# Kernel tuning notes

Hardware: AMD Instinct MI355X
Metric: run time of the kernel (lower is better)

The kernel has to match this reference:

```python
import jax, jax.numpy as jnp
import numpy as np


def _conv1x1(x, w, b=None):
    # x: [B, Cin, N, S], w: [Cout, Cin], 1x1 Conv2d
    y = jnp.einsum('oc,bcns->bons', w, x)
    if b is not None:
        y = y + b[None, :, None, None]
    return y


def setup_inputs() -> dict:
    key = jax.random.key(0)
    ks = jax.random.split(key, 16)
    B, Cin, N, K = 4, 128, 16384, 16
    MID, OUT, SHARE, PT = 64, 128, 8, 10
    s = 0.05
    inp = {
        'sm_feats': jax.random.normal(ks[0], (B, Cin, N, K), jnp.float32),
        'sm_ppfs': jax.random.normal(ks[1], (B, PT, N, K), jnp.float32),
        'conv0_w': jax.random.normal(ks[2], (OUT, Cin), jnp.float32) * s,
        'conv0_b': jax.random.normal(ks[3], (OUT,), jnp.float32) * s,
        'conv1_w': jax.random.normal(ks[4], (MID, OUT), jnp.float32) * s,
        'conv1_b': jax.random.normal(ks[5], (MID,), jnp.float32) * s,
        'conv2_w': jax.random.normal(ks[6], (MID, OUT), jnp.float32) * s,
        'conv2_b': jax.random.normal(ks[7], (MID,), jnp.float32) * s,
        'conv3_w': jax.random.normal(ks[8], (MID, OUT), jnp.float32) * s,
        'conv3_b': jax.random.normal(ks[9], (MID,), jnp.float32) * s,
        'convw1_w': jax.random.normal(ks[10], (MID // SHARE, MID * K), jnp.float32) * s,
        'convw2_w': jax.random.normal(ks[11], (K * MID // SHARE, MID // SHARE), jnp.float32) * s,
        'convw2_b': jax.random.normal(ks[12], (K * MID // SHARE,), jnp.float32) * s,
        'convout_w': jax.random.normal(ks[13], (OUT, MID), jnp.float32) * s,
        'convout_b': jax.random.normal(ks[14], (OUT,), jnp.float32) * s,
        'pt1_w': jax.random.normal(ks[15], (MID, PT), jnp.float32) * s,
        'pt2_w': jax.random.normal(jax.random.fold_in(key, 99), (MID, MID), jnp.float32) * s,
    }
    return inp


def reference(sm_feats, sm_ppfs, conv0_w, conv0_b, conv1_w, conv1_b, conv2_w, conv2_b,
              conv3_w, conv3_b, convw1_w, convw2_w, convw2_b, convout_w, convout_b,
              pt1_w, pt2_w):
    xn = jax.nn.relu(_conv1x1(sm_feats, conv0_w, conv0_b))  # [B, OUT, N, K]
    x = xn[..., :1]                                          # center point feature
    identity = x
    x1 = _conv1x1(x, conv1_w, conv1_b)       # [B, MID, N, 1]
    x2 = _conv1x1(xn, conv2_w, conv2_b)      # [B, MID, N, K]
    x3 = _conv1x1(xn, conv3_w, conv3_b)      # [B, MID, N, K]
    ptf = _conv1x1(jax.nn.relu(_conv1x1(sm_ppfs, pt1_w)), pt2_w)  # [B, MID, N, K]
    x3 = x3 + ptf
    xfs = x1 - x2 + ptf                      # [B, MID, N, K]
    B, MID, N, K = xfs.shape
    share = MID // convw1_w.shape[0]
    xfs = jnp.transpose(xfs, (0, 1, 3, 2)).reshape(B, MID * K, 1, N)
    h = jax.nn.relu(_conv1x1(xfs, convw1_w))            # [B, MID//share, 1, N]
    w = _conv1x1(h, convw2_w, convw2_b)                  # [B, K*MID//share, 1, N]
    w = jax.nn.softmax(w.reshape(B, MID // share, K, N), axis=2)
    w = jnp.transpose(w, (0, 1, 3, 2))                   # [B, MID//share, N, K]
    w = jnp.tile(w, (1, share, 1, 1))                    # [B, MID, N, K]
    out = jax.nn.relu(jnp.sum(w * x3, axis=3, keepdims=True))  # [B, MID, N, 1]
    out = (_conv1x1(out, convout_w, convout_b) + identity).squeeze(3)  # [B, OUT, N]
    return out
```

## Files before the change

kernel.cpp:

```cpp
#include <hip/hip_runtime.h>
#include <hip/hip_bf16.h>


typedef __attribute__((ext_vector_type(8))) short bf16x8;
typedef __attribute__((ext_vector_type(4))) float f32x4;
typedef __attribute__((ext_vector_type(4))) unsigned short us4;

#define MFMA(a, b, c) __builtin_amdgcn_mfma_f32_16x16x32_bf16((a), (b), (c), 0, 0, 0)

#define OFF_F    0
#define OFF_X2   0
#define OFF_PTF  17408
#define OFF_XN   34816
#define OFF_X3   34816
#define OFF_XFS  52224
#define OFF_P    69632
#define OFF_WS   69632
#define OFF_HB   74752
#define OFF_OM   76288
#define OFF_X1   77824
#define OFF_XC   78912
#define SMEM_BYTES 81088

#define WS_W0  0
#define WS_W1  16384
#define WS_W2  24576
#define WS_W3  32768
#define WS_P1  40960
#define WS_P2  43008
#define WS_CW1 47104
#define WS_WO  63488
#define WS_TOTAL 71680

__device__ __forceinline__ unsigned short f2b(float f) {
    union { __hip_bfloat16 h; unsigned short u; } v;
    v.h = __float2bfloat16(f);
    return v.u;
}
__device__ __forceinline__ float b2f(unsigned short u) {
    union { unsigned u; float f; } v;
    v.u = ((unsigned)u) << 16;
    return v.f;
}
__device__ __forceinline__ us4 pk4(float a, float b, float c, float d) {
    us4 r; r[0] = f2b(a); r[1] = f2b(b); r[2] = f2b(c); r[3] = f2b(d); return r;
}
__device__ __forceinline__ bf16x8 ldb(const unsigned short* p) {
    return *(const bf16x8*)p;
}

__global__ __launch_bounds__(512, 1)
void convert_weights(const float* __restrict__ w0, const float* __restrict__ w1,
                     const float* __restrict__ w2, const float* __restrict__ w3,
                     const float* __restrict__ p1, const float* __restrict__ p2,
                     const float* __restrict__ cw1, const float* __restrict__ wo,
                     unsigned short* __restrict__ ws) {
    int i = blockIdx.x * 512 + threadIdx.x;
    if (i >= WS_TOTAL) return;
    float v;
    if (i < 16384)      v = w0[i];
    else if (i < 24576) v = w1[i - 16384];
    else if (i < 32768) v = w2[i - 24576];
    else if (i < 40960) v = w3[i - 32768];
    else if (i < 43008) { int r = i - 40960, row = r >> 5, k = r & 31;
                          v = (k < 10) ? p1[row * 10 + k] : 0.f; }
    else if (i < 47104) v = p2[i - 43008];
    else if (i < 63488) { int r = i - 47104, j = r >> 10, kc = r & 1023;
                          v = (j < 8) ? cw1[j * 1024 + (kc & 63) * 16 + (kc >> 6)] : 0.f; }
    else                v = wo[i - 63488];
    ws[i] = f2b(v);
}

__global__ __launch_bounds__(512, 4)
void fused_model_kernel(const float* __restrict__ feats, const float* __restrict__ ppfs,
                        const unsigned short* __restrict__ wsb,
                        const float* __restrict__ b0, const float* __restrict__ b1,
                        const float* __restrict__ b2, const float* __restrict__ b3,
                        const float* __restrict__ cw2, const float* __restrict__ cb2,
                        const float* __restrict__ bo, float* __restrict__ out) {
    extern __shared__ char smem[];
    const int tid = threadIdx.x;
    const int W = tid >> 6;
    const int lane = tid & 63;
    const int kk = lane & 15;
    const int g = lane >> 4;
    const int bid = blockIdx.x;
    const int b = bid >> 11;
    const int n0 = (bid & 2047) * 8;

    bf16x8 a0[4], rA[4], rB[4];
    {
        const int mtr = (W & 3);
        #pragma unroll
        for (int kt = 0; kt < 4; ++kt) {
            a0[kt] = ldb(wsb + WS_W0 + (16 * W + kk) * 128 + kt * 32 + 8 * g);
            if (W < 4) {
                rA[kt] = ldb(wsb + WS_W3 + (16 * mtr + kk) * 128 + kt * 32 + 8 * g);
                rB[kt] = ldb(wsb + WS_W1 + (16 * mtr + kk) * 128 + kt * 32 + 8 * g);
            } else {
                rA[kt] = ldb(wsb + WS_W2 + (16 * mtr + kk) * 128 + kt * 32 + 8 * g);
                rB[kt] = ldb(wsb + WS_W3 + (16 * mtr + kk) * 128 + kt * 32 + 8 * g);
            }
        }
    }

    {
        const int kq = tid & 3, ci = tid >> 2;
        const int cisw = (ci * 2) ^ (kq << 4);
        #pragma unroll
        for (int pos = 0; pos < 8; ++pos) {
            f32x4 v = *(const f32x4*)(feats + (((size_t)b * 128 + ci) * 16384 + (n0 + pos)) * 16 + kq * 4);
            char* base = smem + OFF_F + pos * 4352 + cisw;
            *(unsigned short*)(base + (kq * 4 + 0) * 272) = f2b(v[0]);
            *(unsigned short*)(base + (kq * 4 + 1) * 272) = f2b(v[1]);
            *(unsigned short*)(base + (kq * 4 + 2) * 272) = f2b(v[2]);
            *(unsigned short*)(base + (kq * 4 + 3) * 272) = f2b(v[3]);
        }
        if (tid < 320) {
            int pos = tid / 40, r = tid % 40, p = r >> 2, kq2 = r & 3;
            f32x4 v = *(const f32x4*)(ppfs + (((size_t)b * 10 + p) * 16384 + (n0 + pos)) * 16 + kq2 * 4);
            char* base = smem + OFF_P + pos * 1024 + p * 2;
            *(unsigned short*)(base + (kq2 * 4 + 0) * 64) = f2b(v[0]);
            *(unsigned short*)(base + (kq2 * 4 + 1) * 64) = f2b(v[1]);
            *(unsigned short*)(base + (kq2 * 4 + 2) * 64) = f2b(v[2]);
            *(unsigned short*)(base + (kq2 * 4 + 3) * 64) = f2b(v[3]);
        } else {
            for (int z = tid - 320; z < 1408; z += 192) {
                int pos = z / 176, rr = z % 176, ks = rr / 11, dw = rr % 11;
                *(unsigned*)(smem + OFF_P + pos * 1024 + ks * 64 + 20 + dw * 4) = 0u;
            }
        }
    }
    __syncthreads();

    {
        f32x4 bv = *(const f32x4*)(b0 + 16 * W + 4 * g);
        const int fsw = ((kk >> 2) & 3) << 4;
        #pragma unroll
        for (int pos = 0; pos < 8; ++pos) {
            f32x4 acc = {0.f, 0.f, 0.f, 0.f};
            #pragma unroll
            for (int kt = 0; kt < 4; ++kt) {
                bf16x8 bf = *(const bf16x8*)(smem + OFF_F + pos * 4352 + kk * 272 + ((kt * 64 + 16 * g) ^ fsw));
                acc = MFMA(a0[kt], bf, acc);
            }
            us4 xw = pk4(fmaxf(acc[0] + bv[0], 0.f), fmaxf(acc[1] + bv[1], 0.f),
                         fmaxf(acc[2] + bv[2], 0.f), fmaxf(acc[3] + bv[3], 0.f));
            *(us4*)(smem + OFF_XN + pos * 4352 + kk * 272 + (16 * W + 4 * g) * 2) = xw;
            if (kk == 0) *(us4*)(smem + OFF_XC + pos * 272 + (16 * W + 4 * g) * 2) = xw;
        }
    }
    __syncthreads();

    f32x4 acc3[4];
    if (W < 4) {
        bf16x8 a1[4], a2[4][2];
        #pragma unroll
        for (int mt = 0; mt < 4; ++mt) {
            a1[mt] = ldb(wsb + WS_P1 + (16 * mt + kk) * 32 + 8 * g);
            a2[mt][0] = ldb(wsb + WS_P2 + (16 * mt + kk) * 64 + 8 * g);
            a2[mt][1] = ldb(wsb + WS_P2 + (16 * mt + kk) * 64 + 32 + 8 * g);
        }
        const int sel = g >> 1;
        const int sa = kk + 16 * ((2 * g) & 3);
        const int sb = kk + 16 * ((2 * g + 1) & 3);
        #pragma unroll
        for (int pp = 0; pp < 2; ++pp) {
            const int pos = 2 * W + pp;
            bf16x8 bp = *(const bf16x8*)(smem + OFF_P + pos * 1024 + kk * 64 + 16 * g);
            int pkd[4][2];
            #pragma unroll
            for (int mt = 0; mt < 4; ++mt) {
                f32x4 hv = {0.f, 0.f, 0.f, 0.f};
                hv = MFMA(a1[mt], bp, hv);
                us4 t = pk4(fmaxf(hv[0], 0.f), fmaxf(hv[1], 0.f),
                            fmaxf(hv[2], 0.f), fmaxf(hv[3], 0.f));
                pkd[mt][0] = ((int*)&t)[0];
                pkd[mt][1] = ((int*)&t)[1];
            }
            union { int d[4]; bf16x8 v; } bh0, bh1;
            bh0.d[0] = sel ? __shfl(pkd[1][0], sa, 64) : __shfl(pkd[0][0], sa, 64);
            bh0.d[1] = sel ? __shfl(pkd[1][1], sa, 64) : __shfl(pkd[0][1], sa, 64);
            bh0.d[2] = sel ? __shfl(pkd[1][0], sb, 64) : __shfl(pkd[0][0], sb, 64);
            bh0.d[3] = sel ? __shfl(pkd[1][1], sb, 64) : __shfl(pkd[0][1], sb, 64);
            bh1.d[0] = sel ? __shfl(pkd[3][0], sa, 64) : __shfl(pkd[2][0], sa, 64);
            bh1.d[1] = sel ? __shfl(pkd[3][1], sa, 64) : __shfl(pkd[2][1], sa, 64);
            bh1.d[2] = sel ? __shfl(pkd[3][0], sb, 64) : __shfl(pkd[2][0], sb, 64);
            bh1.d[3] = sel ? __shfl(pkd[3][1], sb, 64) : __shfl(pkd[2][1], sb, 64);
            #pragma unroll
            for (int mt = 0; mt < 4; ++mt) {
                f32x4 acc = {0.f, 0.f, 0.f, 0.f};
                acc = MFMA(a2[mt][0], bh0.v, acc);
                acc = MFMA(a2[mt][1], bh1.v, acc);
                *(us4*)(smem + OFF_PTF + pos * 2176 + kk * 136 + (16 * mt + 4 * g) * 2) =
                    pk4(acc[0], acc[1], acc[2], acc[3]);
            }
        }
        #pragma unroll
        for (int pp = 0; pp < 4; ++pp) {
            f32x4 acc = {0.f, 0.f, 0.f, 0.f};
            #pragma unroll
            for (int kt = 0; kt < 4; ++kt) {
                bf16x8 bf = *(const bf16x8*)(smem + OFF_XN + pp * 4352 + kk * 272 + (kt * 64 + 16 * g));
                acc = MFMA(rA[kt], bf, acc);
            }
            acc3[pp] = acc;
        }
        f32x4 a1c = {0.f, 0.f, 0.f, 0.f};
        #pragma unroll
        for (int kt = 0; kt < 4; ++kt) {
            bf16x8 bf = *(const bf16x8*)(smem + OFF_XC + (kk & 7) * 272 + (kt * 64 + 16 * g));
            a1c = MFMA(rB[kt], bf, a1c);
        }
        if (kk < 8) {
            f32x4 b1v = *(const f32x4*)(b1 + 16 * W + 4 * g);
            *(us4*)(smem + OFF_X1 + kk * 136 + (16 * W + 4 * g) * 2) =
                pk4(a1c[0] + b1v[0], a1c[1] + b1v[1], a1c[2] + b1v[2], a1c[3] + b1v[3]);
        }
    } else {
        const int mt = W - 4;
        f32x4 b2v = *(const f32x4*)(b2 + 16 * mt + 4 * g);
        #pragma unroll
        for (int pos = 0; pos < 8; ++pos) {
            bf16x8 bx[4];
            #pragma unroll
            for (int kt = 0; kt < 4; ++kt)
                bx[kt] = *(const bf16x8*)(smem + OFF_XN + pos * 4352 + kk * 272 + (kt * 64 + 16 * g));
            f32x4 acc = {0.f, 0.f, 0.f, 0.f};
            #pragma unroll
            for (int kt = 0; kt < 4; ++kt) acc = MFMA(rA[kt], bx[kt], acc);
            *(us4*)(smem + OFF_X2 + pos * 2176 + kk * 136 + (16 * mt + 4 * g) * 2) =
                pk4(acc[0] + b2v[0], acc[1] + b2v[1], acc[2] + b2v[2], acc[3] + b2v[3]);
            if (pos >= 4) {
                f32x4 c = {0.f, 0.f, 0.f, 0.f};
                #pragma unroll
                for (int kt = 0; kt < 4; ++kt) c = MFMA(rB[kt], bx[kt], c);
                acc3[pos - 4] = c;
            }
        }
    }
    __syncthreads();

    {
        const int mt = W & 3, ph = W >> 2;
        f32x4 b3v = *(const f32x4*)(b3 + 16 * mt + 4 * g);
        const int rot = (32 * mt + 8 * g + 16 * kk) & 127;
        #pragma unroll
        for (int pp = 0; pp < 4; ++pp) {
            const int pos = ph * 4 + pp;
            us4 ptfv = *(const us4*)(smem + OFF_PTF + pos * 2176 + kk * 136 + (16 * mt + 4 * g) * 2);
            us4 x2v  = *(const us4*)(smem + OFF_X2  + pos * 2176 + kk * 136 + (16 * mt + 4 * g) * 2);
            us4 x1v  = *(const us4*)(smem + OFF_X1  + pos * 136 + (16 * mt + 4 * g) * 2);
            float pf0 = b2f(ptfv[0]), pf1 = b2f(ptfv[1]), pf2 = b2f(ptfv[2]), pf3 = b2f(ptfv[3]);
            *(us4*)(smem + OFF_X3 + pos * 2176 + kk * 136 + (16 * mt + 4 * g) * 2) =
                pk4(acc3[pp][0] + b3v[0] + pf0, acc3[pp][1] + b3v[1] + pf1,
                    acc3[pp][2] + b3v[2] + pf2, acc3[pp][3] + b3v[3] + pf3);
            *(us4*)(smem + OFF_XFS + pos * 2080 + kk * 128 + rot) =
                pk4(b2f(x1v[0]) - b2f(x2v[0]) + pf0, b2f(x1v[1]) - b2f(x2v[1]) + pf1,
                    b2f(x1v[2]) - b2f(x2v[2]) + pf2, b2f(x1v[3]) - b2f(x2v[3]) + pf3);
        }
        if (tid < 64) *(float*)(smem + OFF_HB + tid * 4) = 0.f;
    }
    __syncthreads();

    {
        bf16x8 acw[4];
        #pragma unroll
        for (int kt = 0; kt < 4; ++kt)
            acw[kt] = ldb(wsb + WS_CW1 + kk * 1024 + W * 128 + kt * 32 + 8 * g);
        const char* xb = smem + OFF_XFS + (kk & 7) * 2080;
        f32x4 acc = {0.f, 0.f, 0.f, 0.f};
        #pragma unroll
        for (int kt = 0; kt < 4; ++kt) {
            const int k = 2 * W + (kt >> 1);
            const int byt = (64 * (kt & 1) + 16 * g + 16 * k) & 127;
            bf16x8 bf = *(const bf16x8*)(xb + k * 128 + byt);
            acc = MFMA(acw[kt], bf, acc);
        }
        if (kk < 8 && g < 2) {
            #pragma unroll
            for (int r = 0; r < 4; ++r)
                atomicAdd((float*)(smem + OFF_HB + kk * 32 + (4 * g + r) * 4), acc[r]);
        }
    }
    __syncthreads();

    {
        const int pos = W;
        f32x4 h0 = *(const f32x4*)(smem + OFF_HB + pos * 32);
        f32x4 h1 = *(const f32x4*)(smem + OFF_HB + pos * 32 + 16);
        #pragma unroll
        for (int r = 0; r < 4; ++r) { h0[r] = fmaxf(h0[r], 0.f); h1[r] = fmaxf(h1[r], 0.f); }
        #pragma unroll
        for (int it = 0; it < 2; ++it) {
            const int c = it * 64 + lane;
            float wl = cb2[c];
            f32x4 w20 = *(const f32x4*)(cw2 + c * 8);
            f32x4 w21 = *(const f32x4*)(cw2 + c * 8 + 4);
            #pragma unroll
            for (int j = 0; j < 4; ++j) {
                wl += w20[j] * h0[j];
                wl += w21[j] * h1[j];
            }
            float mx = wl;
            for (int off = 8; off; off >>= 1) mx = fmaxf(mx, __shfl_xor(mx, off, 16));
            float e = __expf(wl - mx);
            float ss = e;
            for (int off = 8; off; off >>= 1) ss += __shfl_xor(ss, off, 16);
            *(float*)(smem + OFF_WS + pos * 640 + (4 * it + g) * 80 + kk * 4) = e / ss;
        }
        __builtin_amdgcn_wave_barrier();
        __builtin_amdgcn_sched_barrier(0);

        const char* wsp = smem + OFF_WS + pos * 640 + (lane & 7) * 80;
        f32x4 wv0 = *(const f32x4*)(wsp);
        f32x4 wv1 = *(const f32x4*)(wsp + 16);
        f32x4 wv2 = *(const f32x4*)(wsp + 32);
        f32x4 wv3 = *(const f32x4*)(wsp + 48);
        const char* x3b = smem + OFF_X3 + pos * 2176 + lane * 2;
        float s = 0.f;
        #pragma unroll
        for (int k = 0; k < 4; ++k) s += wv0[k] * b2f(*(const unsigned short*)(x3b + k * 136));
        #pragma unroll
        for (int k = 0; k < 4; ++k) s += wv1[k] * b2f(*(const unsigned short*)(x3b + (k + 4) * 136));
        #pragma unroll
        for (int k = 0; k < 4; ++k) s += wv2[k] * b2f(*(const unsigned short*)(x3b + (k + 8) * 136));
        #pragma unroll
        for (int k = 0; k < 4; ++k) s += wv3[k] * b2f(*(const unsigned short*)(x3b + (k + 12) * 136));
        *(unsigned short*)(smem + OFF_OM + pos * 144 + lane * 2) = f2b(fmaxf(s, 0.f));
    }
    __syncthreads();

    {
        f32x4 acc = {0.f, 0.f, 0.f, 0.f};
        #pragma unroll
        for (int kt = 0; kt < 2; ++kt) {
            bf16x8 bf = *(const bf16x8*)(smem + OFF_OM + (kk & 7) * 144 + (kt * 64 + 16 * g));
            acc = MFMA(ldb(wsb + WS_WO + (16 * W + kk) * 64 + kt * 32 + 8 * g), bf, acc);
        }
        if (kk < 8) {
            f32x4 bv = *(const f32x4*)(bo + 16 * W + 4 * g);
            us4 xcv = *(const us4*)(smem + OFF_XC + kk * 272 + (16 * W + 4 * g) * 2);
            #pragma unroll
            for (int r = 0; r < 4; ++r) {
                int o = 16 * W + 4 * g + r;
                out[((size_t)b * 128 + o) * 16384 + n0 + kk] = acc[r] + bv[r] + b2f(xcv[r]);
            }
        }
    }
}

extern "C" void kernel_launch(void* const* d_in, const int* in_sizes, int n_in,
                              void* d_out, int out_size, void* d_ws, size_t ws_size,
                              hipStream_t stream) {
    (void)in_sizes; (void)n_in; (void)out_size; (void)ws_size;
    const float* feats = (const float*)d_in[0];
    const float* ppfs  = (const float*)d_in[1];
    const float* w0  = (const float*)d_in[2];
    const float* b0  = (const float*)d_in[3];
    const float* w1  = (const float*)d_in[4];
    const float* b1  = (const float*)d_in[5];
    const float* w2  = (const float*)d_in[6];
    const float* b2  = (const float*)d_in[7];
    const float* w3  = (const float*)d_in[8];
    const float* b3  = (const float*)d_in[9];
    const float* cw1 = (const float*)d_in[10];
    const float* cw2 = (const float*)d_in[11];
    const float* cb2 = (const float*)d_in[12];
    const float* wo  = (const float*)d_in[13];
    const float* bo  = (const float*)d_in[14];
    const float* p1  = (const float*)d_in[15];
    const float* p2  = (const float*)d_in[16];
    float* out = (float*)d_out;
    unsigned short* wsb = (unsigned short*)d_ws;

    convert_weights<<<dim3((WS_TOTAL + 511) / 512), dim3(512), 0, stream>>>(
        w0, w1, w2, w3, p1, p2, cw1, wo, wsb);

    (void)hipFuncSetAttribute(reinterpret_cast<const void*>(fused_model_kernel),
                              hipFuncAttributeMaxDynamicSharedMemorySize, SMEM_BYTES);
    fused_model_kernel<<<dim3(8192), dim3(512), SMEM_BYTES, stream>>>(
        feats, ppfs, wsb, b0, b1, b2, b3, cw2, cb2, bo, out);
}
```

Before: 303.6 us.

## Make blocks persistent over four tiles with register-prefetched next-tile loads

Each block now handles four consecutive 8-point tiles instead of one, and the grid shrinks from 8192 to 2048 blocks. While the current tile is computed, the feats and ppfs for the next tile are loaded into registers, then written to shared memory after the F buffer is free. This hides global load latency behind compute and amortises the per-block weight register loads. In exchange it raises register pressure (eight extra f32x4 per thread), which may cut occupancy, and leaves fewer blocks to balance across CUs.

Result: slower. 798.2 us (+162.9%).

```diff
diff --git a/kernel.cpp b/kernel.cpp
--- a/kernel.cpp
+++ b/kernel.cpp
@@ -85,8 +85,12 @@
     const int kk = lane & 15;
     const int g = lane >> 4;
     const int bid = blockIdx.x;
-    const int b = bid >> 11;
-    const int n0 = (bid & 2047) * 8;
+    const int b = bid >> 9;
+    const int n0base = (bid & 511) * 32;
+
+    const int kq = tid & 3, ci = tid >> 2;
+    const int cisw = (ci * 2) ^ (kq << 4);
+    const int pposP = tid / 40, rP = tid % 40, pP = rP >> 2, kqP = rP & 3;
 
     bf16x8 a0[4], rA[4], rB[4];
     {
@@ -103,250 +107,278 @@
             }
         }
     }
-
+    f32x4 pf[8];
+    f32x4 pp;
     {
-        const int kq = tid & 3, ci = tid >> 2;
-        const int cisw = (ci * 2) ^ (kq << 4);
+        const float* fb = feats + (((size_t)b * 128 + ci) * 16384 + n0base) * 16 + kq * 4;
         #pragma unroll
-        for (int pos = 0; pos < 8; ++pos) {
-            f32x4 v = *(const f32x4*)(feats + (((size_t)b * 128 + ci) * 16384 + (n0 + pos)) * 16 + kq * 4);
-            char* base = smem + OFF_F + pos * 4352 + cisw;
-            *(unsigned short*)(base + (kq * 4 + 0) * 272) = f2b(v[0]);
-            *(unsigned short*)(base + (kq * 4 + 1) * 272) = f2b(v[1]);
-            *(unsigned short*)(base + (kq * 4 + 2) * 272) = f2b(v[2]);
-            *(unsigned short*)(base + (kq * 4 + 3) * 272) = f2b(v[3]);
-        }
+        for (int pos = 0; pos < 8; ++pos) pf[pos] = *(const f32x4*)(fb + pos * 16);
+        if (tid < 320)
+            pp = *(const f32x4*)(ppfs + (((size_t)b * 10 + pP) * 16384 + n0base + pposP) * 16 + kqP * 4);
+    }
+
+    #pragma unroll 1
+    for (int tt = 0; tt < 4; ++tt) {
+        const int n0 = n0base + tt * 8;
+
         if (tid < 320) {
-            int pos = tid / 40, r = tid % 40, p = r >> 2, kq2 = r & 3;
-            f32x4 v = *(const f32x4*)(ppfs + (((size_t)b * 10 + p) * 16384 + (n0 + pos)) * 16 + kq2 * 4);
-            char* base = smem + OFF_P + pos * 1024 + p * 2;
-            *(unsigned short*)(base + (kq2 * 4 + 0) * 64) = f2b(v[0]);
-            *(unsigned short*)(base + (kq2 * 4 + 1) * 64) = f2b(v[1]);
-            *(unsigned short*)(base + (kq2 * 4 + 2) * 64) = f2b(v[2]);
-            *(unsigned short*)(base + (kq2 * 4 + 3) * 64) = f2b(v[3]);
+            char* basep = smem + OFF_P + pposP * 1024 + pP * 2;
+            *(unsigned short*)(basep + (kqP * 4 + 0) * 64) = f2b(pp[0]);
+            *(unsigned short*)(basep + (kqP * 4 + 1) * 64) = f2b(pp[1]);
+            *(unsigned short*)(basep + (kqP * 4 + 2) * 64) = f2b(pp[2]);
+            *(unsigned short*)(basep + (kqP * 4 + 3) * 64) = f2b(pp[3]);
         } else {
             for (int z = tid - 320; z < 1408; z += 192) {
                 int pos = z / 176, rr = z % 176, ks = rr / 11, dw = rr % 11;
                 *(unsigned*)(smem + OFF_P + pos * 1024 + ks * 64 + 20 + dw * 4) = 0u;
             }
         }
-    }
-    __syncthreads();
-
-    {
-        f32x4 bv = *(const f32x4*)(b0 + 16 * W + 4 * g);
-        const int fsw = ((kk >> 2) & 3) << 4;
-        #pragma unroll
-        for (int pos = 0; pos < 8; ++pos) {
+        if (tt == 0) {
+            #pragma unroll
+            for (int pos = 0; pos < 8; ++pos) {
+                char* base = smem + OFF_F + pos * 4352 + cisw;
+                *(unsigned short*)(base + (kq * 4 + 0) * 272) = f2b(pf[pos][0]);
+                *(unsigned short*)(base + (kq * 4 + 1) * 272) = f2b(pf[pos][1]);
+                *(unsigned short*)(base + (kq * 4 + 2) * 272) = f2b(pf[pos][2]);
+                *(unsigned short*)(base + (kq * 4 + 3) * 272) = f2b(pf[pos][3]);
+            }
+        }
+        if (tt < 3) {
+            const int n1 = n0base + (tt + 1) * 8;
+            const float* fb = feats + (((size_t)b * 128 + ci) * 16384 + n1) * 16 + kq * 4;
+            #pragma unroll
+            for (int pos = 0; pos < 8; ++pos) pf[pos] = *(const f32x4*)(fb + pos * 16);
+            if (tid < 320)
+                pp = *(const f32x4*)(ppfs + (((size_t)b * 10 + pP) * 16384 + n1 + pposP) * 16 + kqP * 4);
+        }
+        if (tt == 0) __syncthreads();
+
+        {
+            f32x4 bv = *(const f32x4*)(b0 + 16 * W + 4 * g);
+            const int fsw = ((kk >> 2) & 3) << 4;
+            #pragma unroll
+            for (int pos = 0; pos < 8; ++pos) {
+                f32x4 acc = {0.f, 0.f, 0.f, 0.f};
+                #pragma unroll
+                for (int kt = 0; kt < 4; ++kt) {
+                    bf16x8 bf = *(const bf16x8*)(smem + OFF_F + pos * 4352 + kk * 272 + ((kt * 64 + 16 * g) ^ fsw));
+                    acc = MFMA(a0[kt], bf, acc);
+                }
+                us4 xw = pk4(fmaxf(acc[0] + bv[0], 0.f), fmaxf(acc[1] + bv[1], 0.f),
+                             fmaxf(acc[2] + bv[2], 0.f), fmaxf(acc[3] + bv[3], 0.f));
+                *(us4*)(smem + OFF_XN + pos * 4352 + kk * 272 + (16 * W + 4 * g) * 2) = xw;
+                if (kk == 0) *(us4*)(smem + OFF_XC + pos * 272 + (16 * W + 4 * g) * 2) = xw;
+            }
+        }
+        __syncthreads();
+
+        f32x4 acc3[4];
+        if (W < 4) {
+            bf16x8 a1[4], a2[4][2];
+            #pragma unroll
+            for (int mt = 0; mt < 4; ++mt) {
+                a1[mt] = ldb(wsb + WS_P1 + (16 * mt + kk) * 32 + 8 * g);
+                a2[mt][0] = ldb(wsb + WS_P2 + (16 * mt + kk) * 64 + 8 * g);
+                a2[mt][1] = ldb(wsb + WS_P2 + (16 * mt + kk) * 64 + 32 + 8 * g);
+            }
+            const int sel = g >> 1;
+            const int sa = kk + 16 * ((2 * g) & 3);
+            const int sb = kk + 16 * ((2 * g + 1) & 3);
+            #pragma unroll
+            for (int pp2 = 0; pp2 < 2; ++pp2) {
+                const int pos = 2 * W + pp2;
+                bf16x8 bp = *(const bf16x8*)(smem + OFF_P + pos * 1024 + kk * 64 + 16 * g);
+                int pkd[4][2];
+                #pragma unroll
+                for (int mt = 0; mt < 4; ++mt) {
+                    f32x4 hv = {0.f, 0.f, 0.f, 0.f};
+                    hv = MFMA(a1[mt], bp, hv);
+                    us4 t = pk4(fmaxf(hv[0], 0.f), fmaxf(hv[1], 0.f),
+                                fmaxf(hv[2], 0.f), fmaxf(hv[3], 0.f));
+                    pkd[mt][0] = ((int*)&t)[0];
+                    pkd[mt][1] = ((int*)&t)[1];
+                }
+                union { int d[4]; bf16x8 v; } bh0, bh1;
+                bh0.d[0] = sel ? __shfl(pkd[1][0], sa, 64) : __shfl(pkd[0][0], sa, 64);
+                bh0.d[1] = sel ? __shfl(pkd[1][1], sa, 64) : __shfl(pkd[0][1], sa, 64);
+                bh0.d[2] = sel ? __shfl(pkd[1][0], sb, 64) : __shfl(pkd[0][0], sb, 64);
+                bh0.d[3] = sel ? __shfl(pkd[1][1], sb, 64) : __shfl(pkd[0][1], sb, 64);
+                bh1.d[0] = sel ? __shfl(pkd[3][0], sa, 64) : __shfl(pkd[2][0], sa, 64);
+                bh1.d[1] = sel ? __shfl(pkd[3][1], sa, 64) : __shfl(pkd[2][1], sa, 64);
+                bh1.d[2] = sel ? __shfl(pkd[3][0], sb, 64) : __shfl(pkd[2][0], sb, 64);
+                bh1.d[3] = sel ? __shfl(pkd[3][1], sb, 64) : __shfl(pkd[2][1], sb, 64);
+                #pragma unroll
+                for (int mt = 0; mt < 4; ++mt) {
+                    f32x4 acc = {0.f, 0.f, 0.f, 0.f};
+                    acc = MFMA(a2[mt][0], bh0.v, acc);
+                    acc = MFMA(a2[mt][1], bh1.v, acc);
+                    *(us4*)(smem + OFF_PTF + pos * 2176 + kk * 136 + (16 * mt + 4 * g) * 2) =
+                        pk4(acc[0], acc[1], acc[2], acc[3]);
+                }
+            }
+            #pragma unroll
+            for (int pp2 = 0; pp2 < 4; ++pp2) {
+                f32x4 acc = {0.f, 0.f, 0.f, 0.f};
+                #pragma unroll
+                for (int kt = 0; kt < 4; ++kt) {
+                    bf16x8 bf = *(const bf16x8*)(smem + OFF_XN + pp2 * 4352 + kk * 272 + (kt * 64 + 16 * g));
+                    acc = MFMA(rA[kt], bf, acc);
+                }
+                acc3[pp2] = acc;
+            }
+            f32x4 a1c = {0.f, 0.f, 0.f, 0.f};
+            #pragma unroll
+            for (int kt = 0; kt < 4; ++kt) {
+                bf16x8 bf = *(const bf16x8*)(smem + OFF_XC + (kk & 7) * 272 + (kt * 64 + 16 * g));
+                a1c = MFMA(rB[kt], bf, a1c);
+            }
+            if (kk < 8) {
+                f32x4 b1v = *(const f32x4*)(b1 + 16 * W + 4 * g);
+                *(us4*)(smem + OFF_X1 + kk * 136 + (16 * W + 4 * g) * 2) =
+                    pk4(a1c[0] + b1v[0], a1c[1] + b1v[1], a1c[2] + b1v[2], a1c[3] + b1v[3]);
+            }
+        } else {
+            const int mt = W - 4;
+            f32x4 b2v = *(const f32x4*)(b2 + 16 * mt + 4 * g);
+            #pragma unroll
+            for (int pos = 0; pos < 8; ++pos) {
+                bf16x8 bx[4];
+                #pragma unroll
+                for (int kt = 0; kt < 4; ++kt)
+                    bx[kt] = *(const bf16x8*)(smem + OFF_XN + pos * 4352 + kk * 272 + (kt * 64 + 16 * g));
+                f32x4 acc = {0.f, 0.f, 0.f, 0.f};
+                #pragma unroll
+                for (int kt = 0; kt < 4; ++kt) acc = MFMA(rA[kt], bx[kt], acc);
+                *(us4*)(smem + OFF_X2 + pos * 2176 + kk * 136 + (16 * mt + 4 * g) * 2) =
+                    pk4(acc[0] + b2v[0], acc[1] + b2v[1], acc[2] + b2v[2], acc[3] + b2v[3]);
+                if (pos >= 4) {
+                    f32x4 c = {0.f, 0.f, 0.f, 0.f};
+                    #pragma unroll
+                    for (int kt = 0; kt < 4; ++kt) c = MFMA(rB[kt], bx[kt], c);
+                    acc3[pos - 4] = c;
+                }
+            }
+        }
+        __syncthreads();
+
+        {
+            const int mt = W & 3, ph = W >> 2;
+            f32x4 b3v = *(const f32x4*)(b3 + 16 * mt + 4 * g);
+            const int rot = (32 * mt + 8 * g + 16 * kk) & 127;
+            #pragma unroll
+            for (int pp2 = 0; pp2 < 4; ++pp2) {
+                const int pos = ph * 4 + pp2;
+                us4 ptfv = *(const us4*)(smem + OFF_PTF + pos * 2176 + kk * 136 + (16 * mt + 4 * g) * 2);
+                us4 x2v  = *(const us4*)(smem + OFF_X2  + pos * 2176 + kk * 136 + (16 * mt + 4 * g) * 2);
+                us4 x1v  = *(const us4*)(smem + OFF_X1  + pos * 136 + (16 * mt + 4 * g) * 2);
+                float pf0 = b2f(ptfv[0]), pf1 = b2f(ptfv[1]), pf2 = b2f(ptfv[2]), pf3 = b2f(ptfv[3]);
+                *(us4*)(smem + OFF_X3 + pos * 2176 + kk * 136 + (16 * mt + 4 * g) * 2) =
+                    pk4(acc3[pp2][0] + b3v[0] + pf0, acc3[pp2][1] + b3v[1] + pf1,
+                        acc3[pp2][2] + b3v[2] + pf2, acc3[pp2][3] + b3v[3] + pf3);
+                *(us4*)(smem + OFF_XFS + pos * 2080 + kk * 128 + rot) =
+                    pk4(b2f(x1v[0]) - b2f(x2v[0]) + pf0, b2f(x1v[1]) - b2f(x2v[1]) + pf1,
+                        b2f(x1v[2]) - b2f(x2v[2]) + pf2, b2f(x1v[3]) - b2f(x2v[3]) + pf3);
+            }
+            if (tid < 64) *(float*)(smem + OFF_HB + tid * 4) = 0.f;
+        }
+        __syncthreads();
+
+        {
+            bf16x8 acw[4];
+            #pragma unroll
+            for (int kt = 0; kt < 4; ++kt)
+                acw[kt] = ldb(wsb + WS_CW1 + kk * 1024 + W * 128 + kt * 32 + 8 * g);
+            const char* xb = smem + OFF_XFS + (kk & 7) * 2080;
             f32x4 acc = {0.f, 0.f, 0.f, 0.f};
             #pragma unroll
             for (int kt = 0; kt < 4; ++kt) {
-                bf16x8 bf = *(const bf16x8*)(smem + OFF_F + pos * 4352 + kk * 272 + ((kt * 64 + 16 * g) ^ fsw));
-                acc = MFMA(a0[kt], bf, acc);
-            }
-            us4 xw = pk4(fmaxf(acc[0] + bv[0], 0.f), fmaxf(acc[1] + bv[1], 0.f),
-                         fmaxf(acc[2] + bv[2], 0.f), fmaxf(acc[3] + bv[3], 0.f));
-            *(us4*)(smem + OFF_XN + pos * 4352 + kk * 272 + (16 * W + 4 * g) * 2) = xw;
-            if (kk == 0) *(us4*)(smem + OFF_XC + pos * 272 + (16 * W + 4 * g) * 2) = xw;
-        }
-    }
-    __syncthreads();
-
-    f32x4 acc3[4];
-    if (W < 4) {
-        bf16x8 a1[4], a2[4][2];
-        #pragma unroll
-        for (int mt = 0; mt < 4; ++mt) {
-            a1[mt] = ldb(wsb + WS_P1 + (16 * mt + kk) * 32 + 8 * g);
-            a2[mt][0] = ldb(wsb + WS_P2 + (16 * mt + kk) * 64 + 8 * g);
-            a2[mt][1] = ldb(wsb + WS_P2 + (16 * mt + kk) * 64 + 32 + 8 * g);
-        }
-        const int sel = g >> 1;
-        const int sa = kk + 16 * ((2 * g) & 3);
-        const int sb = kk + 16 * ((2 * g + 1) & 3);
-        #pragma unroll
-        for (int pp = 0; pp < 2; ++pp) {
-            const int pos = 2 * W + pp;
-            bf16x8 bp = *(const bf16x8*)(smem + OFF_P + pos * 1024 + kk * 64 + 16 * g);
-            int pkd[4][2];
-            #pragma unroll
-            for (int mt = 0; mt < 4; ++mt) {
-                f32x4 hv = {0.f, 0.f, 0.f, 0.f};
-                hv = MFMA(a1[mt], bp, hv);
-                us4 t = pk4(fmaxf(hv[0], 0.f), fmaxf(hv[1], 0.f),
-                            fmaxf(hv[2], 0.f), fmaxf(hv[3], 0.f));
-                pkd[mt][0] = ((int*)&t)[0];
-                pkd[mt][1] = ((int*)&t)[1];
-            }
-            union { int d[4]; bf16x8 v; } bh0, bh1;
-            bh0.d[0] = sel ? __shfl(pkd[1][0], sa, 64) : __shfl(pkd[0][0], sa, 64);
-            bh0.d[1] = sel ? __shfl(pkd[1][1], sa, 64) : __shfl(pkd[0][1], sa, 64);
-            bh0.d[2] = sel ? __shfl(pkd[1][0], sb, 64) : __shfl(pkd[0][0], sb, 64);
-            bh0.d[3] = sel ? __shfl(pkd[1][1], sb, 64) : __shfl(pkd[0][1], sb, 64);
-            bh1.d[0] = sel ? __shfl(pkd[3][0], sa, 64) : __shfl(pkd[2][0], sa, 64);
-            bh1.d[1] = sel ? __shfl(pkd[3][1], sa, 64) : __shfl(pkd[2][1], sa, 64);
-            bh1.d[2] = sel ? __shfl(pkd[3][0], sb, 64) : __shfl(pkd[2][0], sb, 64);
-            bh1.d[3] = sel ? __shfl(pkd[3][1], sb, 64) : __shfl(pkd[2][1], sb, 64);
-            #pragma unroll
-            for (int mt = 0; mt < 4; ++mt) {
-                f32x4 acc = {0.f, 0.f, 0.f, 0.f};
-                acc = MFMA(a2[mt][0], bh0.v, acc);
-                acc = MFMA(a2[mt][1], bh1.v, acc);
-                *(us4*)(smem + OFF_PTF + pos * 2176 + kk * 136 + (16 * mt + 4 * g) * 2) =
-                    pk4(acc[0], acc[1], acc[2], acc[3]);
-            }
-        }
-        #pragma unroll
-        for (int pp = 0; pp < 4; ++pp) {
+                const int k = 2 * W + (kt >> 1);
+                const int byt = (64 * (kt & 1) + 16 * g + 16 * k) & 127;
+                bf16x8 bf = *(const bf16x8*)(xb + k * 128 + byt);
+                acc = MFMA(acw[kt], bf, acc);
+            }
+            if (kk < 8 && g < 2) {
+                #pragma unroll
+                for (int r = 0; r < 4; ++r)
+                    atomicAdd((float*)(smem + OFF_HB + kk * 32 + (4 * g + r) * 4), acc[r]);
+            }
+            if (tt < 3) {
+                #pragma unroll
+                for (int pos = 0; pos < 8; ++pos) {
+                    char* base = smem + OFF_F + pos * 4352 + cisw;
+                    *(unsigned short*)(base + (kq * 4 + 0) * 272) = f2b(pf[pos][0]);
+                    *(unsigned short*)(base + (kq * 4 + 1) * 272) = f2b(pf[pos][1]);
+                    *(unsigned short*)(base + (kq * 4 + 2) * 272) = f2b(pf[pos][2]);
+                    *(unsigned short*)(base + (kq * 4 + 3) * 272) = f2b(pf[pos][3]);
+                }
+            }
+        }
+        __syncthreads();
+
+        {
+            const int pos = W;
+            f32x4 h0 = *(const f32x4*)(smem + OFF_HB + pos * 32);
+            f32x4 h1 = *(const f32x4*)(smem + OFF_HB + pos * 32 + 16);
+            #pragma unroll
+            for (int r = 0; r < 4; ++r) { h0[r] = fmaxf(h0[r], 0.f); h1[r] = fmaxf(h1[r], 0.f); }
+            #pragma unroll
+            for (int it = 0; it < 2; ++it) {
+                const int c = it * 64 + lane;
+                float wl = cb2[c];
+                f32x4 w20 = *(const f32x4*)(cw2 + c * 8);
+                f32x4 w21 = *(const f32x4*)(cw2 + c * 8 + 4);
+                #pragma unroll
+                for (int j = 0; j < 4; ++j) {
+                    wl += w20[j] * h0[j];
+                    wl += w21[j] * h1[j];
+                }
+                float mx = wl;
+                for (int off = 8; off; off >>= 1) mx = fmaxf(mx, __shfl_xor(mx, off, 16));
+                float e = __expf(wl - mx);
+                float ss = e;
+                for (int off = 8; off; off >>= 1) ss += __shfl_xor(ss, off, 16);
+                *(float*)(smem + OFF_WS + pos * 640 + (4 * it + g) * 80 + kk * 4) = e / ss;
+            }
+            __builtin_amdgcn_wave_barrier();
+            __builtin_amdgcn_sched_barrier(0);
+
+            const char* wsp = smem + OFF_WS + pos * 640 + (lane & 7) * 80;
+            f32x4 wv0 = *(const f32x4*)(wsp);
+            f32x4 wv1 = *(const f32x4*)(wsp + 16);
+            f32x4 wv2 = *(const f32x4*)(wsp + 32);
+            f32x4 wv3 = *(const f32x4*)(wsp + 48);
+            const char* x3b = smem + OFF_X3 + pos * 2176 + lane * 2;
+            float s = 0.f;
+            #pragma unroll
+            for (int k = 0; k < 4; ++k) s += wv0[k] * b2f(*(const unsigned short*)(x3b + k * 136));
+            #pragma unroll
+            for (int k = 0; k < 4; ++k) s += wv1[k] * b2f(*(const unsigned short*)(x3b + (k + 4) * 136));
+            #pragma unroll
+            for (int k = 0; k < 4; ++k) s += wv2[k] * b2f(*(const unsigned short*)(x3b + (k + 8) * 136));
+            #pragma unroll
+            for (int k = 0; k < 4; ++k) s += wv3[k] * b2f(*(const unsigned short*)(x3b + (k + 12) * 136));
+            *(unsigned short*)(smem + OFF_OM + pos * 144 + lane * 2) = f2b(fmaxf(s, 0.f));
+        }
+        __syncthreads();
+
+        {
             f32x4 acc = {0.f, 0.f, 0.f, 0.f};
             #pragma unroll
-            for (int kt = 0; kt < 4; ++kt) {
-                bf16x8 bf = *(const bf16x8*)(smem + OFF_XN + pp * 4352 + kk * 272 + (kt * 64 + 16 * g));
-                acc = MFMA(rA[kt], bf, acc);
-            }
-            acc3[pp] = acc;
-        }
-        f32x4 a1c = {0.f, 0.f, 0.f, 0.f};
-        #pragma unroll
-        for (int kt = 0; kt < 4; ++kt) {
-            bf16x8 bf = *(const bf16x8*)(smem + OFF_XC + (kk & 7) * 272 + (kt * 64 + 16 * g));
-            a1c = MFMA(rB[kt], bf, a1c);
-        }
-        if (kk < 8) {
-            f32x4 b1v = *(const f32x4*)(b1 + 16 * W + 4 * g);
-            *(us4*)(smem + OFF_X1 + kk * 136 + (16 * W + 4 * g) * 2) =
-                pk4(a1c[0] + b1v[0], a1c[1] + b1v[1], a1c[2] + b1v[2], a1c[3] + b1v[3]);
-        }
-    } else {
-        const int mt = W - 4;
-        f32x4 b2v = *(const f32x4*)(b2 + 16 * mt + 4 * g);
-        #pragma unroll
-        for (int pos = 0; pos < 8; ++pos) {
-            bf16x8 bx[4];
-            #pragma unroll
-            for (int kt = 0; kt < 4; ++kt)
-                bx[kt] = *(const bf16x8*)(smem + OFF_XN + pos * 4352 + kk * 272 + (kt * 64 + 16 * g));
-            f32x4 acc = {0.f, 0.f, 0.f, 0.f};
-            #pragma unroll
-            for (int kt = 0; kt < 4; ++kt) acc = MFMA(rA[kt], bx[kt], acc);
-            *(us4*)(smem + OFF_X2 + pos * 2176 + kk * 136 + (16 * mt + 4 * g) * 2) =
-                pk4(acc[0] + b2v[0], acc[1] + b2v[1], acc[2] + b2v[2], acc[3] + b2v[3]);
-            if (pos >= 4) {
-                f32x4 c = {0.f, 0.f, 0.f, 0.f};
-                #pragma unroll
-                for (int kt = 0; kt < 4; ++kt) c = MFMA(rB[kt], bx[kt], c);
-                acc3[pos - 4] = c;
-            }
-        }
-    }
-    __syncthreads();
-
-    {
-        const int mt = W & 3, ph = W >> 2;
-        f32x4 b3v = *(const f32x4*)(b3 + 16 * mt + 4 * g);
-        const int rot = (32 * mt + 8 * g + 16 * kk) & 127;
-        #pragma unroll
-        for (int pp = 0; pp < 4; ++pp) {
-            const int pos = ph * 4 + pp;
-            us4 ptfv = *(const us4*)(smem + OFF_PTF + pos * 2176 + kk * 136 + (16 * mt + 4 * g) * 2);
-            us4 x2v  = *(const us4*)(smem + OFF_X2  + pos * 2176 + kk * 136 + (16 * mt + 4 * g) * 2);
-            us4 x1v  = *(const us4*)(smem + OFF_X1  + pos * 136 + (16 * mt + 4 * g) * 2);
-            float pf0 = b2f(ptfv[0]), pf1 = b2f(ptfv[1]), pf2 = b2f(ptfv[2]), pf3 = b2f(ptfv[3]);
-            *(us4*)(smem + OFF_X3 + pos * 2176 + kk * 136 + (16 * mt + 4 * g) * 2) =
-                pk4(acc3[pp][0] + b3v[0] + pf0, acc3[pp][1] + b3v[1] + pf1,
-                    acc3[pp][2] + b3v[2] + pf2, acc3[pp][3] + b3v[3] + pf3);
-            *(us4*)(smem + OFF_XFS + pos * 2080 + kk * 128 + rot) =
-                pk4(b2f(x1v[0]) - b2f(x2v[0]) + pf0, b2f(x1v[1]) - b2f(x2v[1]) + pf1,
-                    b2f(x1v[2]) - b2f(x2v[2]) + pf2, b2f(x1v[3]) - b2f(x2v[3]) + pf3);
-        }
-        if (tid < 64) *(float*)(smem + OFF_HB + tid * 4) = 0.f;
-    }
-    __syncthreads();
-
-    {
-        bf16x8 acw[4];
-        #pragma unroll
-        for (int kt = 0; kt < 4; ++kt)
-            acw[kt] = ldb(wsb + WS_CW1 + kk * 1024 + W * 128 + kt * 32 + 8 * g);
-        const char* xb = smem + OFF_XFS + (kk & 7) * 2080;
-        f32x4 acc = {0.f, 0.f, 0.f, 0.f};
-        #pragma unroll
-        for (int kt = 0; kt < 4; ++kt) {
-            const int k = 2 * W + (kt >> 1);
-            const int byt = (64 * (kt & 1) + 16 * g + 16 * k) & 127;
-            bf16x8 bf = *(const bf16x8*)(xb + k * 128 + byt);
-            acc = MFMA(acw[kt], bf, acc);
-        }
-        if (kk < 8 && g < 2) {
-            #pragma unroll
-            for (int r = 0; r < 4; ++r)
-                atomicAdd((float*)(smem + OFF_HB + kk * 32 + (4 * g + r) * 4), acc[r]);
-        }
-    }
-    __syncthreads();
-
-    {
-        const int pos = W;
-        f32x4 h0 = *(const f32x4*)(smem + OFF_HB + pos * 32);
-        f32x4 h1 = *(const f32x4*)(smem + OFF_HB + pos * 32 + 16);
-        #pragma unroll
-        for (int r = 0; r < 4; ++r) { h0[r] = fmaxf(h0[r], 0.f); h1[r] = fmaxf(h1[r], 0.f); }
-        #pragma unroll
-        for (int it = 0; it < 2; ++it) {
-            const int c = it * 64 + lane;
-            float wl = cb2[c];
-            f32x4 w20 = *(const f32x4*)(cw2 + c * 8);
-            f32x4 w21 = *(const f32x4*)(cw2 + c * 8 + 4);
-            #pragma unroll
-            for (int j = 0; j < 4; ++j) {
-                wl += w20[j] * h0[j];
-                wl += w21[j] * h1[j];
-            }
-            float mx = wl;
-            for (int off = 8; off; off >>= 1) mx = fmaxf(mx, __shfl_xor(mx, off, 16));
-            float e = __expf(wl - mx);
-            float ss = e;
-            for (int off = 8; off; off >>= 1) ss += __shfl_xor(ss, off, 16);
-            *(float*)(smem + OFF_WS + pos * 640 + (4 * it + g) * 80 + kk * 4) = e / ss;
-        }
-        __builtin_amdgcn_wave_barrier();
-        __builtin_amdgcn_sched_barrier(0);
-
-        const char* wsp = smem + OFF_WS + pos * 640 + (lane & 7) * 80;
-        f32x4 wv0 = *(const f32x4*)(wsp);
-        f32x4 wv1 = *(const f32x4*)(wsp + 16);
-        f32x4 wv2 = *(const f32x4*)(wsp + 32);
-        f32x4 wv3 = *(const f32x4*)(wsp + 48);
-        const char* x3b = smem + OFF_X3 + pos * 2176 + lane * 2;
-        float s = 0.f;
-        #pragma unroll
-        for (int k = 0; k < 4; ++k) s += wv0[k] * b2f(*(const unsigned short*)(x3b + k * 136));
-        #pragma unroll
-        for (int k = 0; k < 4; ++k) s += wv1[k] * b2f(*(const unsigned short*)(x3b + (k + 4) * 136));
-        #pragma unroll
-        for (int k = 0; k < 4; ++k) s += wv2[k] * b2f(*(const unsigned short*)(x3b + (k + 8) * 136));
-        #pragma unroll
-        for (int k = 0; k < 4; ++k) s += wv3[k] * b2f(*(const unsigned short*)(x3b + (k + 12) * 136));
-        *(unsigned short*)(smem + OFF_OM + pos * 144 + lane * 2) = f2b(fmaxf(s, 0.f));
-    }
-    __syncthreads();
-
-    {
-        f32x4 acc = {0.f, 0.f, 0.f, 0.f};
-        #pragma unroll
-        for (int kt = 0; kt < 2; ++kt) {
-            bf16x8 bf = *(const bf16x8*)(smem + OFF_OM + (kk & 7) * 144 + (kt * 64 + 16 * g));
-            acc = MFMA(ldb(wsb + WS_WO + (16 * W + kk) * 64 + kt * 32 + 8 * g), bf, acc);
-        }
-        if (kk < 8) {
-            f32x4 bv = *(const f32x4*)(bo + 16 * W + 4 * g);
-            us4 xcv = *(const us4*)(smem + OFF_XC + kk * 272 + (16 * W + 4 * g) * 2);
-            #pragma unroll
-            for (int r = 0; r < 4; ++r) {
-                int o = 16 * W + 4 * g + r;
-                out[((size_t)b * 128 + o) * 16384 + n0 + kk] = acc[r] + bv[r] + b2f(xcv[r]);
-            }
-        }
+            for (int kt = 0; kt < 2; ++kt) {
+                bf16x8 bf = *(const bf16x8*)(smem + OFF_OM + (kk & 7) * 144 + (kt * 64 + 16 * g));
+                acc = MFMA(ldb(wsb + WS_WO + (16 * W + kk) * 64 + kt * 32 + 8 * g), bf, acc);
+            }
+            if (kk < 8) {
+                f32x4 bv = *(const f32x4*)(bo + 16 * W + 4 * g);
+                us4 xcv = *(const us4*)(smem + OFF_XC + kk * 272 + (16 * W + 4 * g) * 2);
+                #pragma unroll
+                for (int r = 0; r < 4; ++r) {
+                    int o = 16 * W + 4 * g + r;
+                    out[((size_t)b * 128 + o) * 16384 + n0 + kk] = acc[r] + bv[r] + b2f(xcv[r]);
+                }
+            }
+        }
+        if (tt != 3) __syncthreads();
     }
 }
 
@@ -379,6 +411,6 @@
 
     (void)hipFuncSetAttribute(reinterpret_cast<const void*>(fused_model_kernel),
                               hipFuncAttributeMaxDynamicSharedMemorySize, SMEM_BYTES);
-    fused_model_kernel<<<dim3(8192), dim3(512), SMEM_BYTES, stream>>>(
+    fused_model_kernel<<<dim3(2048), dim3(512), SMEM_BYTES, stream>>>(
         feats, ppfs, wsb, b0, b1, b2, b3, cw2, cb2, bo, out);
 }
```
